# Performance work log

Measured on AMD Instinct MI355X. Metric: run time of the kernel, lower is better.

The kernel has to match this reference:

```python
import jax, jax.numpy as jnp
import numpy as np

BETA = 0.25
NUM_CODES = 8192
DIM_LATENT = 256
BATCH = 32768


def setup_inputs() -> dict:
    key = jax.random.key(0)
    k1, k2 = jax.random.split(key)
    z_e = jax.random.normal(k1, (BATCH, DIM_LATENT), dtype=jnp.float32)
    # nn.init.uniform_(codebook.weight, -1/num_codes, 1/num_codes)
    codebook = jax.random.uniform(
        k2, (NUM_CODES, DIM_LATENT), dtype=jnp.float32,
        minval=-1.0 / NUM_CODES, maxval=1.0 / NUM_CODES,
    )
    return {"z_e": z_e, "codebook": codebook}


def reference(z_e, codebook):
    # squared L2 distances via the ||z||^2 + ||e||^2 - 2 z.e expansion
    z2 = jnp.sum(z_e * z_e, axis=1, keepdims=True)          # [B, 1]
    e2 = jnp.sum(codebook * codebook, axis=1)[None, :]       # [1, K]
    ze = jnp.einsum('bd,kd->bk', z_e, codebook)              # [B, K]
    dist = z2 + e2 - 2.0 * ze                                # [B, K]
    indices = jnp.argmin(dist, axis=1)                       # [B]
    z_q = codebook[indices]                                  # [B, d] gather

    cb_loss = jnp.mean((z_q - jax.lax.stop_gradient(z_e)) ** 2)
    commit_loss = jnp.mean((z_e - jax.lax.stop_gradient(z_q)) ** 2)
    vq_loss = cb_loss + BETA * commit_loss

    # straight-through estimator
    z_q_st = z_e + jax.lax.stop_gradient(z_q - z_e)
    return (z_q_st, indices, vq_loss, cb_loss, commit_loss)
```

## Files before the change

kernel.cpp:

```cpp
#include <hip/hip_runtime.h>

#define BATCH   32768
#define DIM     256
#define NCODES  8192
#define BETA    0.25f
#define EPS     3e-4f
#define CAND_CAP 128

typedef unsigned short ushort_t;
typedef unsigned char  uchar_t;
typedef unsigned long long u64;
typedef __attribute__((ext_vector_type(8))) short bf16x8;
typedef __attribute__((ext_vector_type(4))) float f32x4;

#define GLOAD16(gp, lp) __builtin_amdgcn_global_load_lds( \
    (const __attribute__((address_space(1))) void*)(gp), \
    (__attribute__((address_space(3))) void*)(lp), 16, 0, 0)

__device__ inline ushort_t f2bf(float f) {
    union { float f; unsigned u; } v; v.f = f;
    return (ushort_t)((v.u + 0x7FFF + ((v.u >> 16) & 1)) >> 16);
}
__device__ inline ushort_t f2bf_rd(float f) {
    union { float f; unsigned u; } v; v.f = f;
    unsigned u = v.u;
    if (f < 0.0f) u += 0xFFFFu;
    return (ushort_t)(u >> 16);
}

__global__ void vq_prep_kernel(const float* __restrict__ z,
                               const float* __restrict__ cb,
                               float* __restrict__ e2, float* __restrict__ z2,
                               ushort_t* __restrict__ eh, ushort_t* __restrict__ zh,
                               float* __restrict__ loss_acc) {
    const int lane = threadIdx.x & 63;
    const int wid  = threadIdx.x >> 6;
    const int item = blockIdx.x * 4 + wid;
    const float* src;
    ushort_t* dst;
    if (item < NCODES) { src = cb + (size_t)item * DIM;            dst = eh + (size_t)item * DIM; }
    else               { src = z  + (size_t)(item - NCODES) * DIM; dst = zh + (size_t)(item - NCODES) * DIM; }
    const float4 v = *(const float4*)(src + lane * 4);
    ushort4 b; b.x = f2bf(v.x); b.y = f2bf(v.y); b.z = f2bf(v.z); b.w = f2bf(v.w);
    *(ushort4*)(dst + lane * 4) = b;
    float s = v.x * v.x + v.y * v.y + v.z * v.z + v.w * v.w;
    #pragma unroll
    for (int off = 32; off > 0; off >>= 1) s += __shfl_down(s, off, 64);
    if (lane == 0) {
        if (item < NCODES) e2[item] = s;
        else               z2[item - NCODES] = s;
    }
    if (blockIdx.x == 0 && threadIdx.x == 0) *loss_acc = 0.0f;
}

__launch_bounds__(256, 2)
__global__ void vq_screen_kernel(const ushort_t* __restrict__ zh_g,
                                 const ushort_t* __restrict__ eh_g,
                                 const float* __restrict__ e2g,
                                 ushort_t* __restrict__ tilemin_g,
                                 uchar_t* __restrict__ mask_g) {
    __shared__ ushort_t zh_s[64 * 32];
    __shared__ ushort_t eh_s[512 * 32];
    __shared__ float    e2_s[512];

    const int t    = threadIdx.x;
    const int w    = t >> 6;
    const int lane = t & 63;
    const int c    = lane & 15;
    const int q    = lane >> 4;
    const int cg   = blockIdx.x & 3;
    const int row0 = (blockIdx.x >> 2) * 64;

    for (int ct2 = 0; ct2 < 4; ++ct2) {
        const int ctg = cg * 4 + ct2;
        __syncthreads();
        e2_s[t]       = e2g[ctg * 512 + t];
        e2_s[256 + t] = e2g[ctg * 512 + 256 + t];

        f32x4 acc[4][8];
        #pragma unroll
        for (int i = 0; i < 4; ++i)
            #pragma unroll
            for (int j = 0; j < 8; ++j) acc[i][j] = (f32x4)0.0f;

        for (int kc = 0; kc < 256; kc += 32) {
            __syncthreads();
            GLOAD16(zh_g + (size_t)(row0 + w * 16 + (lane >> 2)) * DIM + kc + (lane & 3) * 8,
                    &zh_s[w * 512]);
            #pragma unroll
            for (int s8 = 0; s8 < 8; ++s8) {
                const int c16 = w * 8 + s8;
                GLOAD16(eh_g + (size_t)(ctg * 512 + c16 * 16 + (lane >> 2)) * DIM + kc + (lane & 3) * 8,
                        &eh_s[c16 * 512]);
            }
            __syncthreads();

            bf16x8 a[4], b[8];
            #pragma unroll
            for (int i = 0; i < 4; ++i)
                a[i] = *(const bf16x8*)&zh_s[i * 512 + c * 32 + q * 8];
            #pragma unroll
            for (int j = 0; j < 8; ++j)
                b[j] = *(const bf16x8*)&eh_s[(w * 8 + j) * 512 + c * 32 + q * 8];
            #pragma unroll
            for (int i = 0; i < 4; ++i)
                #pragma unroll
                for (int j = 0; j < 8; ++j)
                    acc[i][j] = __builtin_amdgcn_mfma_f32_16x16x32_bf16(a[i], b[j], acc[i][j], 0, 0, 0);
        }

        float tm[4][4];
        #pragma unroll
        for (int i = 0; i < 4; ++i)
            #pragma unroll
            for (int reg = 0; reg < 4; ++reg) tm[i][reg] = 3.4e38f;
        #pragma unroll
        for (int i = 0; i < 4; ++i)
            #pragma unroll
            for (int j = 0; j < 8; ++j) {
                const float e2v = e2_s[w * 128 + j * 16 + c];
                #pragma unroll
                for (int reg = 0; reg < 4; ++reg) {
                    const float s = fmaf(-2.0f, acc[i][j][reg], e2v);
                    acc[i][j][reg] = s;
                    tm[i][reg] = fminf(tm[i][reg], s);
                }
            }
        #pragma unroll
        for (int st = 1; st < 16; st <<= 1)
            #pragma unroll
            for (int i = 0; i < 4; ++i)
                #pragma unroll
                for (int reg = 0; reg < 4; ++reg)
                    tm[i][reg] = fminf(tm[i][reg], __shfl_xor(tm[i][reg], st, 64));

        const int tile = ctg * 4 + w;
        #pragma unroll
        for (int i = 0; i < 4; ++i)
            #pragma unroll
            for (int reg = 0; reg < 4; ++reg) {
                const int row = row0 + i * 16 + q * 4 + reg;
                const float thr = tm[i][reg] + EPS;
                unsigned m8 = 0;
                #pragma unroll
                for (int j = 0; j < 8; ++j)
                    m8 |= (unsigned)(acc[i][j][reg] <= thr) << j;
                mask_g[(size_t)row * 1024 + tile * 16 + c] = (uchar_t)m8;
                if (c == 0) tilemin_g[(size_t)row * 64 + tile] = f2bf_rd(tm[i][reg]);
            }
    }
}

__device__ inline u64 vq_eval(const float* zrow, const float* __restrict__ cb,
                              const float* __restrict__ e2g, float z2v, int code) {
    const float4* z4 = (const float4*)zrow;
    const float4* e4 = (const float4*)(cb + (size_t)code * DIM);
    float acc = 0.0f;
    #pragma unroll 8
    for (int k4 = 0; k4 < DIM / 4; ++k4) {
        const float4 a = z4[k4];
        const float4 b = e4[k4];
        acc = fmaf(a.x, b.x, acc);
        acc = fmaf(a.y, b.y, acc);
        acc = fmaf(a.z, b.z, acc);
        acc = fmaf(a.w, b.w, acc);
    }
    const float S  = z2v + e2g[code];
    const float sc = fmaf(-2.0f, acc, S);
    union { float f; unsigned u; } sb; sb.f = sc;
    return ((u64)sb.u << 32) | (unsigned)code;
}

__global__ void vq_select_kernel(const float* __restrict__ z,
                                 const float* __restrict__ cb,
                                 const float* __restrict__ e2g,
                                 const float* __restrict__ z2g,
                                 const ushort_t* __restrict__ tilemin_g,
                                 const uchar_t* __restrict__ mask_g,
                                 float* __restrict__ idx_f,
                                 int* __restrict__ idx_i) {
    __shared__ float    zrow_s[4][DIM];
    __shared__ ushort_t cand_s[4][CAND_CAP];

    const int lane = threadIdx.x & 63;
    const int w    = threadIdx.x >> 6;
    const int row  = blockIdx.x * 4 + w;

    *(float4*)&zrow_s[w][lane * 4] = *(const float4*)(z + (size_t)row * DIM + lane * 4);

    union { unsigned u; float f; } tv;
    tv.u = ((unsigned)tilemin_g[(size_t)row * 64 + lane]) << 16;
    const float tm = tv.f;
    float gmin = tm;
    #pragma unroll
    for (int d = 32; d > 0; d >>= 1) gmin = fminf(gmin, __shfl_xor(gmin, d, 64));
    const float thr = gmin + EPS;

    u64 m0 = 0, m1 = 0;
    if (tm <= thr) {
        const uchar_t* mb = mask_g + (size_t)row * 1024 + lane * 16;
        m0 = *(const u64*)(mb);
        m1 = *(const u64*)(mb + 8);
    }
    const unsigned cnt = __popcll(m0) + __popcll(m1);
    unsigned inc = cnt;
    #pragma unroll
    for (int d = 1; d < 64; d <<= 1) {
        const unsigned o = __shfl_up(inc, d, 64);
        if (lane >= d) inc += o;
    }
    const unsigned excl  = inc - cnt;
    const unsigned total = __shfl(inc, 63, 64);
    const float z2v = z2g[row];
    u64 best = ~0ull;

    __syncthreads();

    unsigned slot = excl;
    while (m0) {
        const int p = __builtin_ctzll(m0); m0 &= m0 - 1;
        const unsigned code = lane * 128 + (p & 7) * 16 + (p >> 3);
        if (slot < CAND_CAP) cand_s[w][slot] = (ushort_t)code;
        else best = min(best, vq_eval(zrow_s[w], cb, e2g, z2v, (int)code));
        ++slot;
    }
    while (m1) {
        const int p = __builtin_ctzll(m1); m1 &= m1 - 1;
        const unsigned code = lane * 128 + (p & 7) * 16 + 8 + (p >> 3);
        if (slot < CAND_CAP) cand_s[w][slot] = (ushort_t)code;
        else best = min(best, vq_eval(zrow_s[w], cb, e2g, z2v, (int)code));
        ++slot;
    }

    __syncthreads();

    const int n = (int)(total < CAND_CAP ? total : CAND_CAP);
    for (int s = lane; s < n; s += 64)
        best = min(best, vq_eval(zrow_s[w], cb, e2g, z2v, (int)cand_s[w][s]));

    #pragma unroll
    for (int d = 32; d > 0; d >>= 1) {
        const u64 o = (u64)__shfl_xor((unsigned long long)best, d, 64);
        best = min(best, o);
    }
    if (lane == 0) {
        const int k = (int)(best & (u64)(NCODES - 1));
        idx_f[row] = (float)k;
        idx_i[row] = k;
    }
}

__global__ void vq_gather_loss_kernel(const float* __restrict__ z,
                                      const float* __restrict__ cb,
                                      const int* __restrict__ idx_i,
                                      float* __restrict__ zq_out,
                                      float* __restrict__ loss_acc) {
    const int lane = threadIdx.x & 63;
    const int wid  = threadIdx.x >> 6;
    const int row  = blockIdx.x * 4 + wid;
    const int k = idx_i[row];
    const float4 e  = *(const float4*)(cb + (size_t)k * DIM + lane * 4);
    const float4 zv = *(const float4*)(z + (size_t)row * DIM + lane * 4);
    const float dx = e.x - zv.x, dy = e.y - zv.y, dz = e.z - zv.z, dw = e.w - zv.w;
    float4 o;
    o.x = zv.x + dx; o.y = zv.y + dy; o.z = zv.z + dz; o.w = zv.w + dw;
    *(float4*)(zq_out + (size_t)row * DIM + lane * 4) = o;
    float s = dx * dx + dy * dy + dz * dz + dw * dw;
    #pragma unroll
    for (int off = 32; off > 0; off >>= 1) s += __shfl_down(s, off, 64);
    __shared__ float wsum[4];
    if (lane == 0) wsum[wid] = s;
    __syncthreads();
    if (threadIdx.x == 0)
        atomicAdd(loss_acc, wsum[0] + wsum[1] + wsum[2] + wsum[3]);
}

__global__ void vq_finalize_kernel(const float* __restrict__ loss_acc,
                                   float* __restrict__ out_losses) {
    const float mean = *loss_acc * (1.0f / (float)(BATCH * DIM));
    out_losses[0] = mean + BETA * mean;
    out_losses[1] = mean;
    out_losses[2] = mean;
}

extern "C" void kernel_launch(void* const* d_in, const int* in_sizes, int n_in,
                              void* d_out, int out_size, void* d_ws, size_t ws_size,
                              hipStream_t stream) {
    const float* z  = (const float*)d_in[0];
    const float* cb = (const float*)d_in[1];

    float* out    = (float*)d_out;
    float* zq     = out;
    float* idx_f  = out + (size_t)BATCH * DIM;
    float* losses = out + (size_t)BATCH * DIM + BATCH;
    uchar_t* mask = (uchar_t*)d_out;

    float*    ws        = (float*)d_ws;
    float*    loss_acc  = ws;
    float*    e2        = ws + 256;
    float*    z2        = e2 + NCODES;
    ushort_t* tilemin   = (ushort_t*)(z2 + BATCH);
    int*      idxi      = (int*)(tilemin + (size_t)BATCH * 64);
    ushort_t* zh        = (ushort_t*)(idxi + BATCH);
    ushort_t* eh        = zh + (size_t)BATCH * DIM;

    vq_prep_kernel<<<(NCODES + BATCH) / 4, 256, 0, stream>>>(z, cb, e2, z2, eh, zh, loss_acc);
    vq_screen_kernel<<<(BATCH / 64) * 4, 256, 0, stream>>>(zh, eh, e2, tilemin, mask);
    vq_select_kernel<<<BATCH / 4, 256, 0, stream>>>(z, cb, e2, z2, tilemin, mask, idx_f, idxi);
    vq_gather_loss_kernel<<<BATCH / 4, 256, 0, stream>>>(z, cb, idxi, zq, loss_acc);
    vq_finalize_kernel<<<1, 1, 0, stream>>>(loss_acc, losses);
}
```

Baseline: 547.3 us.

## Double-buffer screen kernel LDS loads and cover all codes per row block

The screen kernel now double-buffers the bf16 z and codebook tiles in shared memory. It issues the global-to-LDS loads for the next k-chunk before running the MFMAs on the current one, so there is one barrier per step instead of two. Each block now walks all 16 code tiles for its 64 rows rather than splitting codes across 4 blocks, which cuts the grid to a quarter. e2 is read straight from global memory instead of being staged in shared memory. This doubles LDS use per block and may lower occupancy, and the smaller grid could leave the GPU less evenly loaded.

```diff
diff --git a/kernel.cpp b/kernel.cpp
--- a/kernel.cpp
+++ b/kernel.cpp
@@ -59,96 +59,105 @@
                                  const float* __restrict__ e2g,
                                  ushort_t* __restrict__ tilemin_g,
                                  uchar_t* __restrict__ mask_g) {
-    __shared__ ushort_t zh_s[64 * 32];
-    __shared__ ushort_t eh_s[512 * 32];
-    __shared__ float    e2_s[512];
+    __shared__ ushort_t zh_s[2][64 * 32];
+    __shared__ ushort_t eh_s[2][512 * 32];
 
     const int t    = threadIdx.x;
     const int w    = t >> 6;
     const int lane = t & 63;
     const int c    = lane & 15;
     const int q    = lane >> 4;
-    const int cg   = blockIdx.x & 3;
-    const int row0 = (blockIdx.x >> 2) * 64;
-
-    for (int ct2 = 0; ct2 < 4; ++ct2) {
-        const int ctg = cg * 4 + ct2;
+    const int row0 = blockIdx.x * 64;
+
+    const size_t zh_base = (size_t)(row0 + w * 16 + (lane >> 2)) * DIM + (lane & 3) * 8;
+    const size_t eh_base = (size_t)((lane >> 2)) * DIM + (lane & 3) * 8;
+
+    #define STAGE(n_, b_) do {                                              \
+        const int ct_ = (n_) >> 3;                                          \
+        const int kc_ = ((n_) & 7) * 32;                                    \
+        GLOAD16(zh_g + zh_base + kc_, &zh_s[b_][w * 512]);                  \
+        _Pragma("unroll")                                                   \
+        for (int s8_ = 0; s8_ < 8; ++s8_) {                                 \
+            const int c16_ = w * 8 + s8_;                                   \
+            GLOAD16(eh_g + eh_base + (size_t)(ct_ * 512 + c16_ * 16) * DIM + kc_, \
+                    &eh_s[b_][c16_ * 512]);                                 \
+        }                                                                   \
+    } while (0)
+
+    STAGE(0, 0);
+
+    f32x4 acc[4][8];
+    for (int n = 0; n < 128; ++n) {
+        const int kc_i = n & 7;
+        if (kc_i == 0) {
+            #pragma unroll
+            for (int i = 0; i < 4; ++i)
+                #pragma unroll
+                for (int j = 0; j < 8; ++j) acc[i][j] = (f32x4)0.0f;
+        }
         __syncthreads();
-        e2_s[t]       = e2g[ctg * 512 + t];
-        e2_s[256 + t] = e2g[ctg * 512 + 256 + t];
-
-        f32x4 acc[4][8];
+        if (n < 127) STAGE(n + 1, (n + 1) & 1);
+        const int b = n & 1;
+
+        bf16x8 a[4], bfr[8];
         #pragma unroll
         for (int i = 0; i < 4; ++i)
-            #pragma unroll
-            for (int j = 0; j < 8; ++j) acc[i][j] = (f32x4)0.0f;
-
-        for (int kc = 0; kc < 256; kc += 32) {
-            __syncthreads();
-            GLOAD16(zh_g + (size_t)(row0 + w * 16 + (lane >> 2)) * DIM + kc + (lane & 3) * 8,
-                    &zh_s[w * 512]);
-            #pragma unroll
-            for (int s8 = 0; s8 < 8; ++s8) {
-                const int c16 = w * 8 + s8;
-                GLOAD16(eh_g + (size_t)(ctg * 512 + c16 * 16 + (lane >> 2)) * DIM + kc + (lane & 3) * 8,
-                        &eh_s[c16 * 512]);
-            }
-            __syncthreads();
-
-            bf16x8 a[4], b[8];
-            #pragma unroll
-            for (int i = 0; i < 4; ++i)
-                a[i] = *(const bf16x8*)&zh_s[i * 512 + c * 32 + q * 8];
-            #pragma unroll
-            for (int j = 0; j < 8; ++j)
-                b[j] = *(const bf16x8*)&eh_s[(w * 8 + j) * 512 + c * 32 + q * 8];
-            #pragma unroll
-            for (int i = 0; i < 4; ++i)
-                #pragma unroll
-                for (int j = 0; j < 8; ++j)
-                    acc[i][j] = __builtin_amdgcn_mfma_f32_16x16x32_bf16(a[i], b[j], acc[i][j], 0, 0, 0);
-        }
-
-        float tm[4][4];
+            a[i] = *(const bf16x8*)&zh_s[b][i * 512 + c * 32 + q * 8];
+        #pragma unroll
+        for (int j = 0; j < 8; ++j)
+            bfr[j] = *(const bf16x8*)&eh_s[b][(w * 8 + j) * 512 + c * 32 + q * 8];
         #pragma unroll
         for (int i = 0; i < 4; ++i)
             #pragma unroll
-            for (int reg = 0; reg < 4; ++reg) tm[i][reg] = 3.4e38f;
-        #pragma unroll
-        for (int i = 0; i < 4; ++i)
-            #pragma unroll
-            for (int j = 0; j < 8; ++j) {
-                const float e2v = e2_s[w * 128 + j * 16 + c];
+            for (int j = 0; j < 8; ++j)
+                acc[i][j] = __builtin_amdgcn_mfma_f32_16x16x32_bf16(a[i], bfr[j], acc[i][j], 0, 0, 0);
+
+        if (kc_i == 7) {
+            const int ct = n >> 3;
+            float e2v[8];
+            #pragma unroll
+            for (int j = 0; j < 8; ++j) e2v[j] = e2g[ct * 512 + w * 128 + j * 16 + c];
+
+            float tm[4][4];
+            #pragma unroll
+            for (int i = 0; i < 4; ++i)
+                #pragma unroll
+                for (int reg = 0; reg < 4; ++reg) tm[i][reg] = 3.4e38f;
+            #pragma unroll
+            for (int i = 0; i < 4; ++i)
+                #pragma unroll
+                for (int j = 0; j < 8; ++j)
+                    #pragma unroll
+                    for (int reg = 0; reg < 4; ++reg) {
+                        const float s = fmaf(-2.0f, acc[i][j][reg], e2v[j]);
+                        acc[i][j][reg] = s;
+                        tm[i][reg] = fminf(tm[i][reg], s);
+                    }
+            #pragma unroll
+            for (int st = 1; st < 16; st <<= 1)
+                #pragma unroll
+                for (int i = 0; i < 4; ++i)
+                    #pragma unroll
+                    for (int reg = 0; reg < 4; ++reg)
+                        tm[i][reg] = fminf(tm[i][reg], __shfl_xor(tm[i][reg], st, 64));
+
+            const int tile = ct * 4 + w;
+            #pragma unroll
+            for (int i = 0; i < 4; ++i)
                 #pragma unroll
                 for (int reg = 0; reg < 4; ++reg) {
-                    const float s = fmaf(-2.0f, acc[i][j][reg], e2v);
-                    acc[i][j][reg] = s;
-                    tm[i][reg] = fminf(tm[i][reg], s);
+                    const int row = row0 + i * 16 + q * 4 + reg;
+                    const float thr = tm[i][reg] + EPS;
+                    unsigned m8 = 0;
+                    #pragma unroll
+                    for (int j = 0; j < 8; ++j)
+                        m8 |= (unsigned)(acc[i][j][reg] <= thr) << j;
+                    mask_g[(size_t)row * 1024 + tile * 16 + c] = (uchar_t)m8;
+                    if (c == 0) tilemin_g[(size_t)row * 64 + tile] = f2bf_rd(tm[i][reg]);
                 }
-            }
-        #pragma unroll
-        for (int st = 1; st < 16; st <<= 1)
-            #pragma unroll
-            for (int i = 0; i < 4; ++i)
-                #pragma unroll
-                for (int reg = 0; reg < 4; ++reg)
-                    tm[i][reg] = fminf(tm[i][reg], __shfl_xor(tm[i][reg], st, 64));
-
-        const int tile = ctg * 4 + w;
-        #pragma unroll
-        for (int i = 0; i < 4; ++i)
-            #pragma unroll
-            for (int reg = 0; reg < 4; ++reg) {
-                const int row = row0 + i * 16 + q * 4 + reg;
-                const float thr = tm[i][reg] + EPS;
-                unsigned m8 = 0;
-                #pragma unroll
-                for (int j = 0; j < 8; ++j)
-                    m8 |= (unsigned)(acc[i][j][reg] <= thr) << j;
-                mask_g[(size_t)row * 1024 + tile * 16 + c] = (uchar_t)m8;
-                if (c == 0) tilemin_g[(size_t)row * 64 + tile] = f2bf_rd(tm[i][reg]);
-            }
-    }
+        }
+    }
+    #undef STAGE
 }
 
 __device__ inline u64 vq_eval(const float* zrow, const float* __restrict__ cb,
@@ -305,7 +314,7 @@
     ushort_t* eh        = zh + (size_t)BATCH * DIM;
 
     vq_prep_kernel<<<(NCODES + BATCH) / 4, 256, 0, stream>>>(z, cb, e2, z2, eh, zh, loss_acc);
-    vq_screen_kernel<<<(BATCH / 64) * 4, 256, 0, stream>>>(zh, eh, e2, tilemin, mask);
+    vq_screen_kernel<<<BATCH / 64, 256, 0, stream>>>(zh, eh, e2, tilemin, mask);
     vq_select_kernel<<<BATCH / 4, 256, 0, stream>>>(z, cb, e2, z2, tilemin, mask, idx_f, idxi);
     vq_gather_loss_kernel<<<BATCH / 4, 256, 0, stream>>>(z, cb, idxi, zq, loss_acc);
     vq_finalize_kernel<<<1, 1, 0, stream>>>(loss_acc, losses);
```

After: 499.0 us. -8.8%, faster.
